# Kernel tuning notes

Measured on AMD Instinct MI355X. Metric: run time of the kernel, lower is better.

The kernel has to match this reference:

```python
import jax, jax.numpy as jnp
import numpy as np

BN_EPS = 1e-5


def setup_inputs() -> dict:
    key = jax.random.key(0)
    ks = jax.random.split(key, 6)
    n, c, h, w = 16, 256, 80, 80
    mip = max(8, c // 32)  # reduction=32 -> mip=8
    x = jax.random.normal(ks[0], (n, c, h, w), dtype=jnp.float32)
    # 1x1 conv weights (bias=False), stored as [out_ch, in_ch]
    w_fc = jax.random.normal(ks[1], (mip, c), dtype=jnp.float32) * (1.0 / np.sqrt(c))
    w_h = jax.random.normal(ks[2], (c, mip), dtype=jnp.float32) * (1.0 / np.sqrt(mip))
    w_w = jax.random.normal(ks[3], (c, mip), dtype=jnp.float32) * (1.0 / np.sqrt(mip))
    # BatchNorm2d(mip) inference params
    bn_gamma = jnp.ones((mip,), dtype=jnp.float32)
    bn_beta = jnp.zeros((mip,), dtype=jnp.float32)
    bn_mean = jax.random.normal(ks[4], (mip,), dtype=jnp.float32) * 0.1
    bn_var = jax.random.uniform(ks[5], (mip,), dtype=jnp.float32, minval=0.5, maxval=1.5)
    return {"x": x, "w_fc": w_fc, "bn_gamma": bn_gamma, "bn_beta": bn_beta,
            "bn_mean": bn_mean, "bn_var": bn_var, "w_h": w_h, "w_w": w_w}


def reference(x, w_fc, bn_gamma, bn_beta, bn_mean, bn_var, w_h, w_w):
    n, c, h, w = x.shape
    # Adaptive pools: pool_h -> mean over W (n,c,h); pool_w -> mean over H (n,c,w)
    x_h = jnp.mean(x, axis=3)  # (n, c, h)
    x_w = jnp.mean(x, axis=2)  # (n, c, w)
    # concat along the length axis (equiv. to torch cat on dim=2 after permute)
    y = jnp.concatenate([x_h, x_w], axis=2)  # (n, c, h+w)
    # fc: 1x1 conv c->mip + BN (inference) + SiLU
    y = jnp.einsum('mc,ncl->nml', w_fc, y)  # (n, mip, h+w)
    inv = bn_gamma / jnp.sqrt(bn_var + BN_EPS)
    y = y * inv[None, :, None] + (bn_beta - bn_mean * inv)[None, :, None]
    y = y * jax.nn.sigmoid(y)  # SiLU
    y_h, y_w = y[:, :, :h], y[:, :, h:]  # (n, mip, h), (n, mip, w)
    a_h = jax.nn.sigmoid(jnp.einsum('cm,nml->ncl', w_h, y_h))  # (n, c, h)
    a_w = jax.nn.sigmoid(jnp.einsum('cm,nml->ncl', w_w, y_w))  # (n, c, w)
    return x * a_h[:, :, :, None] * a_w[:, :, None, :]
```

## Files before the change

### kernel.cpp

```cpp
#include <hip/hip_runtime.h>

#define N_   16
#define C_   256
#define H_   80
#define W_   80
#define MIP_ 8
#define L_   160

typedef float f32x4 __attribute__((ext_vector_type(4)));

__global__ __launch_bounds__(256) void pool_kernel(const float* __restrict__ x,
                                                   float* __restrict__ pooled) {
    __shared__ float lds[H_ * 81];
    const int b = blockIdx.x;
    const int t = threadIdx.x;

    const float4* pv = reinterpret_cast<const float4*>(x + (size_t)b * (H_ * W_));
    #pragma unroll
    for (int it = 0; it < 7; ++it) {
        int v = t + it * 256;
        if (v < 1600) {
            float4 q = pv[v];
            int row  = v / 20;
            int col0 = (v - row * 20) * 4;
            float* dst = &lds[row * 81 + col0];
            dst[0] = q.x; dst[1] = q.y; dst[2] = q.z; dst[3] = q.w;
        }
    }
    __syncthreads();

    float* outp = pooled + (size_t)b * L_;
    if (t < H_) {
        float s0 = 0.f, s1 = 0.f, s2 = 0.f, s3 = 0.f;
        const float* r = &lds[t * 81];
        #pragma unroll
        for (int c4 = 0; c4 < W_; c4 += 4) {
            s0 += r[c4]; s1 += r[c4 + 1]; s2 += r[c4 + 2]; s3 += r[c4 + 3];
        }
        outp[t] = (s0 + s1 + s2 + s3) * (1.0f / (float)W_);
    } else if (t >= 128 && t < 128 + W_) {
        const int j = t - 128;
        float s0 = 0.f, s1 = 0.f, s2 = 0.f, s3 = 0.f;
        #pragma unroll
        for (int r4 = 0; r4 < H_; r4 += 4) {
            s0 += lds[(r4    ) * 81 + j];
            s1 += lds[(r4 + 1) * 81 + j];
            s2 += lds[(r4 + 2) * 81 + j];
            s3 += lds[(r4 + 3) * 81 + j];
        }
        outp[H_ + j] = (s0 + s1 + s2 + s3) * (1.0f / (float)H_);
    }
}

__global__ __launch_bounds__(256) void mid_kernel(const float* __restrict__ pooled,
                                                  const float* __restrict__ w_fc,
                                                  const float* __restrict__ g,
                                                  const float* __restrict__ be,
                                                  const float* __restrict__ mu,
                                                  const float* __restrict__ va,
                                                  float* __restrict__ y_out) {
    __shared__ float red[4 * MIP_];
    const int b    = blockIdx.x;
    const int n    = b / L_;
    const int l    = b - n * L_;
    const int c    = threadIdx.x;
    const int lane = c & 63;
    const int wid  = c >> 6;

    const float p = pooled[((size_t)n * C_ + c) * L_ + l];

    #pragma unroll
    for (int m = 0; m < MIP_; ++m) {
        float v = w_fc[m * C_ + c] * p;
        #pragma unroll
        for (int off = 32; off > 0; off >>= 1) v += __shfl_down(v, off, 64);
        if (lane == 0) red[wid * MIP_ + m] = v;
    }
    __syncthreads();

    if (c < MIP_) {
        float y   = red[c] + red[MIP_ + c] + red[2 * MIP_ + c] + red[3 * MIP_ + c];
        float inv = g[c] * rsqrtf(va[c] + 1e-5f);
        y = y * inv + (be[c] - mu[c] * inv);
        y_out[(size_t)b * MIP_ + c] = y / (1.0f + expf(-y));
    }
}

__global__ __launch_bounds__(256) void apply_kernel(const float* __restrict__ x,
                                                    const float* __restrict__ y,
                                                    const float* __restrict__ w_h,
                                                    const float* __restrict__ w_w,
                                                    float* __restrict__ out) {
    __shared__ float lah[4][H_];
    __shared__ float law[4][W_];
    const int b  = blockIdx.x;
    const int n  = b >> 6;
    const int c0 = (b & 63) << 2;
    const int t  = threadIdx.x;

    #pragma unroll
    for (int pass = 0; pass < 3; ++pass) {
        int idx = t + pass * 256;
        if (idx < 4 * L_) {
            int ch = idx / L_;
            int l  = idx - ch * L_;
            int c  = c0 + ch;
            const float4* yp = reinterpret_cast<const float4*>(y + ((size_t)n * L_ + l) * MIP_);
            const float4* wp = reinterpret_cast<const float4*>(((l < H_) ? w_h : w_w) + c * MIP_);
            float4 y0 = yp[0], y1 = yp[1];
            float4 w0 = wp[0], w1 = wp[1];
            float s = y0.x * w0.x + y0.y * w0.y + y0.z * w0.z + y0.w * w0.w
                    + y1.x * w1.x + y1.y * w1.y + y1.z * w1.z + y1.w * w1.w;
            float gate = 1.0f / (1.0f + expf(-s));
            if (l < H_) lah[ch][l] = gate; else law[ch][l - H_] = gate;
        }
    }
    __syncthreads();

    const float4* xv = reinterpret_cast<const float4*>(x + ((size_t)n * C_ + c0) * (H_ * W_));
    f32x4*        ov = reinterpret_cast<f32x4*>(out + ((size_t)n * C_ + c0) * (H_ * W_));
    #pragma unroll
    for (int it = 0; it < 25; ++it) {
        int v     = t + it * 256;
        int plane = v / 1600;
        int vv    = v - plane * 1600;
        int row   = vv / 20;
        int col0  = (vv - row * 20) * 4;
        float4 q  = xv[v];
        const float ah = lah[plane][row];
        const float* lw = &law[plane][col0];
        f32x4 o;
        o.x = q.x * ah * lw[0];
        o.y = q.y * ah * lw[1];
        o.z = q.z * ah * lw[2];
        o.w = q.w * ah * lw[3];
        __builtin_nontemporal_store(o, &ov[v]);
    }
}

extern "C" void kernel_launch(void* const* d_in, const int* in_sizes, int n_in,
                              void* d_out, int out_size, void* d_ws, size_t ws_size,
                              hipStream_t stream) {
    const float* x    = (const float*)d_in[0];
    const float* w_fc = (const float*)d_in[1];
    const float* g    = (const float*)d_in[2];
    const float* be   = (const float*)d_in[3];
    const float* mu   = (const float*)d_in[4];
    const float* va   = (const float*)d_in[5];
    const float* w_h  = (const float*)d_in[6];
    const float* w_w  = (const float*)d_in[7];
    float* out = (float*)d_out;

    float* pooled = (float*)d_ws;
    float* y      = pooled + (size_t)N_ * C_ * L_;

    pool_kernel <<<N_ * C_,     256, 0, stream>>>(x, pooled);
    mid_kernel  <<<N_ * L_,     256, 0, stream>>>(pooled, w_fc, g, be, mu, va, y);
    apply_kernel<<<N_ * C_ / 4, 256, 0, stream>>>(x, y, w_h, w_w, out);
}
```

Before: 220.9 us.

## Fuse pool, mid and apply into one cooperative kernel holding x in registers

Replaces the three launches with a single cooperative kernel of 512 blocks, each owning 8 channel planes. Each block loads its slice of x into registers once, pools it through LDS, and synchronises the whole grid twice: once to compute the fc/BN/SiLU stage and once to apply the gates from the same registers. This removes the second full read of x and two kernel launch boundaries. In exchange it needs about 200 VGPRs per thread for the register tile, with a spill risk, and runs at low occupancy. Pooling is serialised plane by plane with block barriers and grid-wide syncs. If the cooperative launch fails, it falls back to the old three-kernel path.

```diff
diff --git a/kernel.cpp b/kernel.cpp
--- a/kernel.cpp
+++ b/kernel.cpp
@@ -1,4 +1,5 @@
 #include <hip/hip_runtime.h>
+#include <hip/hip_cooperative_groups.h>
 
 #define N_   16
 #define C_   256
@@ -9,12 +10,149 @@
 
 typedef float f32x4 __attribute__((ext_vector_type(4)));
 
+namespace cg = cooperative_groups;
+
+__global__ __launch_bounds__(256, 2) void fused_kernel(
+    const float* __restrict__ x,
+    const float* __restrict__ w_fc,
+    const float* __restrict__ g,
+    const float* __restrict__ be,
+    const float* __restrict__ mu,
+    const float* __restrict__ va,
+    const float* __restrict__ w_h,
+    const float* __restrict__ w_w,
+    float* __restrict__ pooled_t,
+    float* __restrict__ y_glob,
+    float* __restrict__ out)
+{
+    __shared__ float smem[H_ * 81];
+    float* lah = smem;
+    float* law = smem + 8 * H_;
+    float* red = smem + 16 * H_;
+
+    const int b    = blockIdx.x;
+    const int n    = b >> 5;
+    const int c0   = (b & 31) << 3;
+    const int t    = threadIdx.x;
+    const int wv   = t >> 6;
+    const int lane = t & 63;
+
+    const f32x4* xv = reinterpret_cast<const f32x4*>(x + ((size_t)n * C_ + c0) * (H_ * W_));
+    f32x4 qx[50];
+    #pragma unroll
+    for (int j = 0; j < 50; ++j)
+        qx[j] = xv[wv * 3200 + 64 * j + lane];
+
+    #pragma unroll
+    for (int p = 0; p < 8; ++p) {
+        if (wv == (p >> 1)) {
+            const int jb = (p & 1) * 25;
+            #pragma unroll
+            for (int k = 0; k < 25; ++k) {
+                int o    = lane + 64 * k;
+                int row  = o / 20;
+                int col0 = (o - row * 20) * 4;
+                float* dst = &smem[row * 81 + col0];
+                f32x4 q = qx[jb + k];
+                dst[0] = q.x; dst[1] = q.y; dst[2] = q.z; dst[3] = q.w;
+            }
+        }
+        __syncthreads();
+        const int c = c0 + p;
+        if (t < H_) {
+            float s0 = 0.f, s1 = 0.f, s2 = 0.f, s3 = 0.f;
+            const float* r = &smem[t * 81];
+            #pragma unroll
+            for (int c4 = 0; c4 < W_; c4 += 4) {
+                s0 += r[c4]; s1 += r[c4 + 1]; s2 += r[c4 + 2]; s3 += r[c4 + 3];
+            }
+            pooled_t[((size_t)n * L_ + t) * C_ + c] = (s0 + s1 + s2 + s3) * (1.0f / (float)W_);
+        } else if (t >= 128 && t < 128 + W_) {
+            const int j2 = t - 128;
+            float s0 = 0.f, s1 = 0.f, s2 = 0.f, s3 = 0.f;
+            #pragma unroll
+            for (int r4 = 0; r4 < H_; r4 += 4) {
+                s0 += smem[(r4    ) * 81 + j2];
+                s1 += smem[(r4 + 1) * 81 + j2];
+                s2 += smem[(r4 + 2) * 81 + j2];
+                s3 += smem[(r4 + 3) * 81 + j2];
+            }
+            pooled_t[((size_t)n * L_ + H_ + j2) * C_ + c] = (s0 + s1 + s2 + s3) * (1.0f / (float)H_);
+        }
+        __syncthreads();
+    }
+
+    cg::this_grid().sync();
+
+    {
+        float wfr[MIP_];
+        #pragma unroll
+        for (int m = 0; m < MIP_; ++m) wfr[m] = w_fc[m * C_ + t];
+        #pragma unroll
+        for (int i = 0; i < 5; ++i) {
+            const int pair = b * 5 + i;
+            const int np   = pair / L_;
+            const int lp   = pair - np * L_;
+            const float pch = pooled_t[((size_t)np * L_ + lp) * C_ + t];
+            #pragma unroll
+            for (int m = 0; m < MIP_; ++m) {
+                float v = wfr[m] * pch;
+                #pragma unroll
+                for (int off = 32; off > 0; off >>= 1) v += __shfl_down(v, off, 64);
+                if (lane == 0) red[wv * MIP_ + m] = v;
+            }
+            __syncthreads();
+            if (t < MIP_) {
+                float s   = red[t] + red[MIP_ + t] + red[2 * MIP_ + t] + red[3 * MIP_ + t];
+                float inv = g[t] * rsqrtf(va[t] + 1e-5f);
+                s = s * inv + (be[t] - mu[t] * inv);
+                y_glob[(size_t)pair * MIP_ + t] = s / (1.0f + expf(-s));
+            }
+            __syncthreads();
+        }
+    }
+
+    cg::this_grid().sync();
+
+    if (t < L_) {
+        const f32x4* yp = reinterpret_cast<const f32x4*>(y_glob + ((size_t)n * L_ + t) * MIP_);
+        f32x4 ya = yp[0], yb = yp[1];
+        const float* wbase = (t < H_) ? w_h : w_w;
+        #pragma unroll
+        for (int ch = 0; ch < 8; ++ch) {
+            const f32x4* wp = reinterpret_cast<const f32x4*>(wbase + (size_t)(c0 + ch) * MIP_);
+            f32x4 w0 = wp[0], w1 = wp[1];
+            float s = ya.x * w0.x + ya.y * w0.y + ya.z * w0.z + ya.w * w0.w
+                    + yb.x * w1.x + yb.y * w1.y + yb.z * w1.z + yb.w * w1.w;
+            float gate = 1.0f / (1.0f + expf(-s));
+            if (t < H_) lah[ch * H_ + t]        = gate;
+            else        law[ch * W_ + (t - H_)] = gate;
+        }
+    }
+    __syncthreads();
+
+    f32x4* ovb = reinterpret_cast<f32x4*>(out + ((size_t)n * C_ + c0) * (H_ * W_));
+    #pragma unroll
+    for (int j = 0; j < 50; ++j) {
+        const int q25   = (j >= 25) ? 1 : 0;
+        const int o     = lane + 64 * (j - 25 * q25);
+        const int plane = 2 * wv + q25;
+        const int row   = o / 20;
+        const int col4  = o - row * 20;
+        const float gr  = lah[plane * H_ + row];
+        const f32x4 gc  = *reinterpret_cast<const f32x4*>(&law[plane * W_ + col4 * 4]);
+        f32x4 q = qx[j], r;
+        r.x = q.x * gr * gc.x; r.y = q.y * gr * gc.y;
+        r.z = q.z * gr * gc.z; r.w = q.w * gr * gc.w;
+        __builtin_nontemporal_store(r, &ovb[wv * 3200 + 64 * j + lane]);
+    }
+}
+
 __global__ __launch_bounds__(256) void pool_kernel(const float* __restrict__ x,
                                                    float* __restrict__ pooled) {
     __shared__ float lds[H_ * 81];
     const int b = blockIdx.x;
     const int t = threadIdx.x;
-
     const float4* pv = reinterpret_cast<const float4*>(x + (size_t)b * (H_ * W_));
     #pragma unroll
     for (int it = 0; it < 7; ++it) {
@@ -28,7 +166,6 @@
         }
     }
     __syncthreads();
-
     float* outp = pooled + (size_t)b * L_;
     if (t < H_) {
         float s0 = 0.f, s1 = 0.f, s2 = 0.f, s3 = 0.f;
@@ -66,9 +203,7 @@
     const int c    = threadIdx.x;
     const int lane = c & 63;
     const int wid  = c >> 6;
-
     const float p = pooled[((size_t)n * C_ + c) * L_ + l];
-
     #pragma unroll
     for (int m = 0; m < MIP_; ++m) {
         float v = w_fc[m * C_ + c] * p;
@@ -77,7 +212,6 @@
         if (lane == 0) red[wid * MIP_ + m] = v;
     }
     __syncthreads();
-
     if (c < MIP_) {
         float y   = red[c] + red[MIP_ + c] + red[2 * MIP_ + c] + red[3 * MIP_ + c];
         float inv = g[c] * rsqrtf(va[c] + 1e-5f);
@@ -97,7 +231,6 @@
     const int n  = b >> 6;
     const int c0 = (b & 63) << 2;
     const int t  = threadIdx.x;
-
     #pragma unroll
     for (int pass = 0; pass < 3; ++pass) {
         int idx = t + pass * 256;
@@ -116,7 +249,6 @@
         }
     }
     __syncthreads();
-
     const float4* xv = reinterpret_cast<const float4*>(x + ((size_t)n * C_ + c0) * (H_ * W_));
     f32x4*        ov = reinterpret_cast<f32x4*>(out + ((size_t)n * C_ + c0) * (H_ * W_));
     #pragma unroll
@@ -149,12 +281,18 @@
     const float* va   = (const float*)d_in[5];
     const float* w_h  = (const float*)d_in[6];
     const float* w_w  = (const float*)d_in[7];
-    float* out = (float*)d_out;
-
+    float* out    = (float*)d_out;
     float* pooled = (float*)d_ws;
     float* y      = pooled + (size_t)N_ * C_ * L_;
 
-    pool_kernel <<<N_ * C_,     256, 0, stream>>>(x, pooled);
-    mid_kernel  <<<N_ * L_,     256, 0, stream>>>(pooled, w_fc, g, be, mu, va, y);
-    apply_kernel<<<N_ * C_ / 4, 256, 0, stream>>>(x, y, w_h, w_w, out);
-}
+    void* args[] = { (void*)&x, (void*)&w_fc, (void*)&g, (void*)&be, (void*)&mu,
+                     (void*)&va, (void*)&w_h, (void*)&w_w,
+                     (void*)&pooled, (void*)&y, (void*)&out };
+    hipError_t err = hipLaunchCooperativeKernel((const void*)fused_kernel,
+                                                dim3(512), dim3(256), args, 0, stream);
+    if (err != hipSuccess) {
+        pool_kernel <<<N_ * C_,     256, 0, stream>>>(x, pooled);
+        mid_kernel  <<<N_ * L_,     256, 0, stream>>>(pooled, w_fc, g, be, mu, va, y);
+        apply_kernel<<<N_ * C_ / 4, 256, 0, stream>>>(x, y, w_h, w_w, out);
+    }
+}
```

Result: slower. 354.3 us (+60.4%).
